# Kernel tuning notes

Measured on AMD Instinct MI355X. Metric: run time of the kernel, lower is better.

## Reference

```python
import jax, jax.numpy as jnp
import numpy as np

N = 50000
E = 800000
DIM_IN = 128
DIM_H = 16
HEADS = 8
DIM_OUT = 16
NEG_SLOPE = 0.2


def setup_inputs() -> dict:
    key = jax.random.key(0)
    ks = jax.random.split(key, 12)
    def glorot(k, shape):
        fan_in = shape[0]
        return jax.random.normal(k, shape, dtype=jnp.float32) / np.sqrt(fan_in)
    x = jax.random.normal(ks[0], (N, DIM_IN), dtype=jnp.float32)
    edge_index = jax.random.randint(ks[1], (2, E), 0, N, dtype=jnp.int64)
    # layer 1: GATv2Conv(dim_in, dim_h, heads=8)
    Wl1 = glorot(ks[2], (DIM_IN, HEADS * DIM_H))
    Wr1 = glorot(ks[3], (DIM_IN, HEADS * DIM_H))
    att1 = glorot(ks[4], (HEADS, DIM_H))
    bias1 = jnp.zeros((HEADS * DIM_H,), dtype=jnp.float32)
    # layer 2: GATv2Conv(dim_h*heads, dim_out, heads=1)
    Wl2 = glorot(ks[5], (HEADS * DIM_H, DIM_OUT))
    Wr2 = glorot(ks[6], (HEADS * DIM_H, DIM_OUT))
    att2 = glorot(ks[7], (1, DIM_OUT))
    bias2 = jnp.zeros((DIM_OUT,), dtype=jnp.float32)
    return {"x": x, "edge_index": edge_index, "Wl1": Wl1, "Wr1": Wr1,
            "att1": att1, "bias1": bias1, "Wl2": Wl2, "Wr2": Wr2,
            "att2": att2, "bias2": bias2}


def gatv2_layer(x, src, dst, Wl, Wr, att, bias, n_nodes, heads, ch):
    # x: [N, F_in]; src/dst: [Etot] (self-loops included)
    xl = (x @ Wl).reshape(n_nodes, heads, ch)  # source transform
    xr = (x @ Wr).reshape(n_nodes, heads, ch)  # target transform
    e = jax.nn.leaky_relu(xl[src] + xr[dst], NEG_SLOPE)      # [Etot, H, C]
    logits = jnp.einsum('ehc,hc->eh', e, att)                # [Etot, H]
    # segment softmax over incoming edges of each target node
    m = jax.ops.segment_max(logits, dst, num_segments=n_nodes)
    a = jnp.exp(logits - m[dst])
    denom = jax.ops.segment_sum(a, dst, num_segments=n_nodes)
    alpha = a / denom[dst]                                   # [Etot, H]
    out = jax.ops.segment_sum(xl[src] * alpha[:, :, None], dst,
                              num_segments=n_nodes)          # [N, H, C]
    return out.reshape(n_nodes, heads * ch) + bias


def reference(x, edge_index, Wl1, Wr1, att1, bias1, Wl2, Wr2, att2, bias2):
    # PyG GATv2Conv adds self-loops by default
    loops = jnp.arange(N, dtype=edge_index.dtype)
    src = jnp.concatenate([edge_index[0], loops])
    dst = jnp.concatenate([edge_index[1], loops])
    # dropout is identity in eval mode
    h = gatv2_layer(x, src, dst, Wl1, Wr1, att1, bias1, N, HEADS, DIM_H)
    h = jax.nn.elu(h)
    h = gatv2_layer(h, src, dst, Wl2, Wr2, att2, bias2, N, 1, DIM_OUT)
    return h, jax.nn.log_softmax(h, axis=1)
```

## Files before the change

### kernel.cpp

```cpp
#include <hip/hip_runtime.h>
#include <hip/hip_bf16.h>
#include <math.h>

#define NN 50000
#define EE 800000
#define DIN 128
#define HEADS 8
#define DH 16
#define DOUT 16
#define NEG 0.2f
#define GM 32
#define GB ((NN + GM - 1) / GM)
#define NB ((NN + 255) / 256)
#define DEGB ((EE / 4 + 255) / 256)
#define NPART 8
#define RANGE (NN / NPART)
#define FILLB (DEGB * NPART)
#define PAD 64

typedef __attribute__((ext_vector_type(8))) short bf16x8;
typedef __attribute__((ext_vector_type(4))) float f32x4;
typedef __attribute__((ext_vector_type(4))) int i32x4;

__device__ __forceinline__ unsigned pack2bf(float a, float b) {
    union { __hip_bfloat162 h; unsigned u; } c;
    c.h = __float22bfloat162_rn(make_float2(a, b));
    return c.u;
}
__device__ __forceinline__ unsigned short f2bf(float v) {
    union { __hip_bfloat16 h; unsigned short u; } c;
    c.h = __float2bfloat16(v);
    return c.u;
}
__device__ __forceinline__ float bflo(unsigned u) { return __uint_as_float(u << 16); }
__device__ __forceinline__ float bfhi(unsigned u) { return __uint_as_float(u & 0xffff0000u); }

__global__ __launch_bounds__(256) void init_wcvt(int* __restrict__ cnt,
                                                 unsigned short* __restrict__ esrcPad,
                                                 const float* __restrict__ Wl,
                                                 const float* __restrict__ Wr,
                                                 unsigned short* __restrict__ Wb,
                                                 const float* __restrict__ Wl2,
                                                 const float* __restrict__ Wr2,
                                                 unsigned short* __restrict__ Wb2) {
    int b = blockIdx.x, t = threadIdx.x;
    if (b < NB) {
        int i = b * 256 + t;
        if (i < NN) {
            cnt[i] = 1;
            esrcPad[(size_t)i * PAD] = (unsigned short)i;
        }
    } else if (b < NB + 128) {
        int i = (b - NB) * 256 + t;
        int n = i >> 7, k = i & 127;
        float v = (n < 128) ? Wl[k * 128 + n] : Wr[k * 128 + (n - 128)];
        Wb[i] = f2bf(v);
    } else {
        int i = (b - NB - 128) * 256 + t;
        int n = i >> 7, k = i & 127;
        float v = (n < 16) ? Wl2[k * 16 + n] : Wr2[k * 16 + (n - 16)];
        Wb2[i] = f2bf(v);
    }
}

__global__ __launch_bounds__(256) void fill_gemm1(const int* __restrict__ ei,
                                                  int* __restrict__ cnt,
                                                  unsigned short* __restrict__ esrcPad,
                                                  const float* __restrict__ x,
                                                  const unsigned short* __restrict__ Wb,
                                                  unsigned short* __restrict__ xlb,
                                                  float* __restrict__ xr) {
    __shared__ unsigned short As[GM][136];
    int t = threadIdx.x;
    if (blockIdx.x < FILLB) {
        int chunk = blockIdx.x >> 3;
        int r = blockIdx.x & 7;
        int i = chunk * 256 + t;
        if (i >= EE / 4) return;
        i32x4 ss = __builtin_nontemporal_load(((const i32x4*)ei) + i);
        i32x4 dd = __builtin_nontemporal_load(((const i32x4*)(ei + EE)) + i);
        int lo = r * RANGE;
        int p;
        if ((unsigned)(dd[0] - lo) < RANGE) {
            p = atomicAdd(&cnt[dd[0]], 1);
            esrcPad[(size_t)dd[0] * PAD + p] = (unsigned short)ss[0];
        }
        if ((unsigned)(dd[1] - lo) < RANGE) {
            p = atomicAdd(&cnt[dd[1]], 1);
            esrcPad[(size_t)dd[1] * PAD + p] = (unsigned short)ss[1];
        }
        if ((unsigned)(dd[2] - lo) < RANGE) {
            p = atomicAdd(&cnt[dd[2]], 1);
            esrcPad[(size_t)dd[2] * PAD + p] = (unsigned short)ss[2];
        }
        if ((unsigned)(dd[3] - lo) < RANGE) {
            p = atomicAdd(&cnt[dd[3]], 1);
            esrcPad[(size_t)dd[3] * PAD + p] = (unsigned short)ss[3];
        }
        return;
    }
    int n0 = (blockIdx.x - FILLB) * GM;
    {
        int row = t >> 3, seg = t & 7;
        int nsrc = n0 + row < NN ? n0 + row : NN - 1;
        const f32x4* xp = (const f32x4*)(x + (size_t)nsrc * DIN + 16 * seg);
        f32x4 v0 = __builtin_nontemporal_load(xp);
        f32x4 v1 = __builtin_nontemporal_load(xp + 1);
        f32x4 v2 = __builtin_nontemporal_load(xp + 2);
        f32x4 v3 = __builtin_nontemporal_load(xp + 3);
        uint4 p0 = make_uint4(pack2bf(v0[0], v0[1]), pack2bf(v0[2], v0[3]),
                              pack2bf(v1[0], v1[1]), pack2bf(v1[2], v1[3]));
        uint4 p1 = make_uint4(pack2bf(v2[0], v2[1]), pack2bf(v2[2], v2[3]),
                              pack2bf(v3[0], v3[1]), pack2bf(v3[2], v3[3]));
        *(uint4*)&As[row][16 * seg]     = p0;
        *(uint4*)&As[row][16 * seg + 8] = p1;
    }
    __syncthreads();
    int lane = t & 63, w = t >> 6;
    int m = lane & 15, quad = lane >> 4;
    f32x4 acc[2][4];
#pragma unroll
    for (int mt = 0; mt < 2; ++mt)
#pragma unroll
        for (int nt = 0; nt < 4; ++nt) acc[mt][nt] = (f32x4){0.f, 0.f, 0.f, 0.f};
#pragma unroll
    for (int ks = 0; ks < 4; ++ks) {
        int k = 32 * ks + 8 * quad;
        bf16x8 a0 = *(const bf16x8*)&As[m][k];
        bf16x8 a1 = *(const bf16x8*)&As[16 + m][k];
#pragma unroll
        for (int nt = 0; nt < 4; ++nt) {
            int n = 64 * w + 16 * nt + m;
            bf16x8 b = *(const bf16x8*)(Wb + (size_t)n * 128 + k);
            acc[0][nt] = __builtin_amdgcn_mfma_f32_16x16x32_bf16(a0, b, acc[0][nt], 0, 0, 0);
            acc[1][nt] = __builtin_amdgcn_mfma_f32_16x16x32_bf16(a1, b, acc[1][nt], 0, 0, 0);
        }
    }
#pragma unroll
    for (int mt = 0; mt < 2; ++mt) {
#pragma unroll
        for (int nt = 0; nt < 4; ++nt) {
            int col = 64 * w + 16 * nt + m;
            int rbase = n0 + 16 * mt + 4 * quad;
            if (col < 128) {
#pragma unroll
                for (int r = 0; r < 4; ++r) {
                    int row = rbase + r;
                    if (row < NN) xlb[(size_t)row * DIN + col] = f2bf(acc[mt][nt][r]);
                }
            } else {
#pragma unroll
                for (int r = 0; r < 4; ++r) {
                    int row = rbase + r;
                    if (row < NN) xr[(size_t)row * DIN + (col - 128)] = acc[mt][nt][r];
                }
            }
        }
    }
}

__global__ __launch_bounds__(256) void l1_fused(const unsigned short* __restrict__ esrcPad,
                                                const int* __restrict__ cnt,
                                                const unsigned short* __restrict__ xlb,
                                                const float* __restrict__ xr,
                                                const float* __restrict__ att,
                                                const float* __restrict__ bias,
                                                unsigned short* __restrict__ hb) {
    int d = blockIdx.x * 4 + (threadIdx.x >> 6);
    int lane = threadIdx.x & 63;
    int quarter = lane >> 4;
    int q16 = lane & 15;
    int rs = d * PAD;
    int re = rs + cnt[d];
    int last = re - 1;
    float4 xr0 = ((const float4*)(xr + (size_t)d * DIN))[2 * q16];
    float4 xr1 = ((const float4*)(xr + (size_t)d * DIN))[2 * q16 + 1];
    float4 at0 = ((const float4*)att)[2 * q16];
    float4 at1 = ((const float4*)att)[2 * q16 + 1];
    float4 a0 = make_float4(0.f, 0.f, 0.f, 0.f);
    float4 a1 = make_float4(0.f, 0.f, 0.f, 0.f);
    float l = 0.f;
    int slot = rs + quarter;
    int c0 = slot < last ? slot : last;
    int s0 = esrcPad[c0];
    int c1 = slot + 4 < last ? slot + 4 : last;
    int s1 = esrcPad[c1];
    uint4 row = ((const uint4*)(xlb + (size_t)s0 * DIN))[q16];
    for (; slot < re; slot += 4) {
        uint4 cur = row;
        int c2 = slot + 8 < last ? slot + 8 : last;
        int s2 = esrcPad[c2];
        row = ((const uint4*)(xlb + (size_t)s1 * DIN))[q16];
        s1 = s2;
        float f0 = bflo(cur.x), f1 = bfhi(cur.x);
        float f2 = bflo(cur.y), f3 = bfhi(cur.y);
        float f4 = bflo(cur.z), f5 = bfhi(cur.z);
        float f6 = bflo(cur.w), f7 = bfhi(cur.w);
        float v0 = f0 + xr0.x; v0 = fmaxf(v0, NEG * v0);
        float v1 = f1 + xr0.y; v1 = fmaxf(v1, NEG * v1);
        float v2 = f2 + xr0.z; v2 = fmaxf(v2, NEG * v2);
        float v3 = f3 + xr0.w; v3 = fmaxf(v3, NEG * v3);
        float v4 = f4 + xr1.x; v4 = fmaxf(v4, NEG * v4);
        float v5 = f5 + xr1.y; v5 = fmaxf(v5, NEG * v5);
        float v6 = f6 + xr1.z; v6 = fmaxf(v6, NEG * v6);
        float v7 = f7 + xr1.w; v7 = fmaxf(v7, NEG * v7);
        float w = at0.x * v0 + at0.y * v1 + at0.z * v2 + at0.w * v3
                + at1.x * v4 + at1.y * v5 + at1.z * v6 + at1.w * v7;
        w += __shfl_xor(w, 1);
        float p = __expf(w);
        a0.x += p * f0; a0.y += p * f1; a0.z += p * f2; a0.w += p * f3;
        a1.x += p * f4; a1.y += p * f5; a1.z += p * f6; a1.w += p * f7;
        l += p;
    }
#pragma unroll
    for (int off = 16; off < 64; off <<= 1) {
        a0.x += __shfl_xor(a0.x, off); a0.y += __shfl_xor(a0.y, off);
        a0.z += __shfl_xor(a0.z, off); a0.w += __shfl_xor(a0.w, off);
        a1.x += __shfl_xor(a1.x, off); a1.y += __shfl_xor(a1.y, off);
        a1.z += __shfl_xor(a1.z, off); a1.w += __shfl_xor(a1.w, off);
        l += __shfl_xor(l, off);
    }
    if (quarter == 0) {
        float inv = 1.f / l;
        float4 b0 = ((const float4*)bias)[2 * q16];
        float4 b1 = ((const float4*)bias)[2 * q16 + 1];
        float4 o0, o1;
        o0.x = a0.x * inv + b0.x; o0.x = o0.x > 0.f ? o0.x : expm1f(o0.x);
        o0.y = a0.y * inv + b0.y; o0.y = o0.y > 0.f ? o0.y : expm1f(o0.y);
        o0.z = a0.z * inv + b0.z; o0.z = o0.z > 0.f ? o0.z : expm1f(o0.z);
        o0.w = a0.w * inv + b0.w; o0.w = o0.w > 0.f ? o0.w : expm1f(o0.w);
        o1.x = a1.x * inv + b1.x; o1.x = o1.x > 0.f ? o1.x : expm1f(o1.x);
        o1.y = a1.y * inv + b1.y; o1.y = o1.y > 0.f ? o1.y : expm1f(o1.y);
        o1.z = a1.z * inv + b1.z; o1.z = o1.z > 0.f ? o1.z : expm1f(o1.z);
        o1.w = a1.w * inv + b1.w; o1.w = o1.w > 0.f ? o1.w : expm1f(o1.w);
        uint4 pk = make_uint4(pack2bf(o0.x, o0.y), pack2bf(o0.z, o0.w),
                              pack2bf(o1.x, o1.y), pack2bf(o1.z, o1.w));
        ((uint4*)(hb + (size_t)d * DIN))[q16] = pk;
    }
}

__global__ __launch_bounds__(256) void gemm2(const unsigned short* __restrict__ hb,
                                             const unsigned short* __restrict__ Wb2,
                                             float* __restrict__ xl2, float* __restrict__ xr2) {
    __shared__ unsigned short As[GM][136];
    int t = threadIdx.x;
    int n0 = blockIdx.x * GM;
    {
        int row = t >> 3, s8 = t & 7;
        int nsrc = n0 + row < NN ? n0 + row : NN - 1;
        const uint4* src = (const uint4*)(hb + (size_t)nsrc * DIN);
        *(uint4*)&As[row][8 * s8]      = src[s8];
        *(uint4*)&As[row][8 * s8 + 64] = src[s8 + 8];
    }
    __syncthreads();
    int lane = t & 63, w = t >> 6;
    int m = lane & 15, quad = lane >> 4;
    int mt = w & 1, nt = w >> 1;
    f32x4 acc = (f32x4){0.f, 0.f, 0.f, 0.f};
#pragma unroll
    for (int ks = 0; ks < 4; ++ks) {
        int k = 32 * ks + 8 * quad;
        bf16x8 a = *(const bf16x8*)&As[16 * mt + m][k];
        bf16x8 b = *(const bf16x8*)(Wb2 + (size_t)(16 * nt + m) * 128 + k);
        acc = __builtin_amdgcn_mfma_f32_16x16x32_bf16(a, b, acc, 0, 0, 0);
    }
    float* __restrict__ dst = (nt == 0) ? xl2 : xr2;
#pragma unroll
    for (int r = 0; r < 4; ++r) {
        int node = n0 + 16 * mt + 4 * quad + r;
        if (node < NN) dst[(size_t)node * DOUT + m] = acc[r];
    }
}

__global__ __launch_bounds__(256) void l2_fused(const unsigned short* __restrict__ esrcPad,
                                                const int* __restrict__ cnt,
                                                const float* __restrict__ xl,
                                                const float* __restrict__ xr,
                                                const float* __restrict__ att,
                                                const float* __restrict__ bias,
                                                float* __restrict__ out) {
    int d = blockIdx.x * 4 + (threadIdx.x >> 6);
    int lane = threadIdx.x & 63;
    int sl = lane >> 2;
    int q = lane & 3;
    int rs = d * PAD;
    int re = rs + cnt[d];
    int last = re - 1;
    float4 xrq = ((const float4*)(xr + (size_t)d * DOUT))[q];
    float4 atq = ((const float4*)att)[q];
    float4 acc = make_float4(0.f, 0.f, 0.f, 0.f);
    float l = 0.f;
    int slot = rs + sl;
    int c0 = slot < last ? slot : last;
    int s0 = esrcPad[c0];
    for (; slot < re; slot += 16) {
        int c1 = slot + 16 < last ? slot + 16 : last;
        int s1 = esrcPad[c1];
        float4 cur = ((const float4*)(xl + (size_t)s0 * DOUT))[q];
        s0 = s1;
        float v0 = cur.x + xrq.x; v0 = fmaxf(v0, NEG * v0);
        float v1 = cur.y + xrq.y; v1 = fmaxf(v1, NEG * v1);
        float v2 = cur.z + xrq.z; v2 = fmaxf(v2, NEG * v2);
        float v3 = cur.w + xrq.w; v3 = fmaxf(v3, NEG * v3);
        float w = atq.x * v0 + atq.y * v1 + atq.z * v2 + atq.w * v3;
        w += __shfl_xor(w, 1);
        w += __shfl_xor(w, 2);
        float p = __expf(w);
        acc.x += p * cur.x; acc.y += p * cur.y;
        acc.z += p * cur.z; acc.w += p * cur.w;
        l += p;
    }
#pragma unroll
    for (int off = 4; off < 64; off <<= 1) {
        acc.x += __shfl_xor(acc.x, off);
        acc.y += __shfl_xor(acc.y, off);
        acc.z += __shfl_xor(acc.z, off);
        acc.w += __shfl_xor(acc.w, off);
        l += __shfl_xor(l, off);
    }
    float inv = 1.f / l;
    float4 b = ((const float4*)bias)[q];
    float4 v;
    v.x = acc.x * inv + b.x; v.y = acc.y * inv + b.y;
    v.z = acc.z * inv + b.z; v.w = acc.w * inv + b.w;
    float m = fmaxf(fmaxf(v.x, v.y), fmaxf(v.z, v.w));
    m = fmaxf(m, __shfl_xor(m, 1));
    m = fmaxf(m, __shfl_xor(m, 2));
    float es = __expf(v.x - m) + __expf(v.y - m) + __expf(v.z - m) + __expf(v.w - m);
    es += __shfl_xor(es, 1);
    es += __shfl_xor(es, 2);
    float lse = m + __logf(es);
    if (sl == 0) {
        ((float4*)(out + (size_t)d * DOUT))[q] = v;
        float4 ls;
        ls.x = v.x - lse; ls.y = v.y - lse; ls.z = v.z - lse; ls.w = v.w - lse;
        ((float4*)(out + (size_t)NN * DOUT + (size_t)d * DOUT))[q] = ls;
    }
}

extern "C" void kernel_launch(void* const* d_in, const int* in_sizes, int n_in,
                              void* d_out, int out_size, void* d_ws, size_t ws_size,
                              hipStream_t stream) {
    const float* x     = (const float*)d_in[0];
    const int*   ei    = (const int*)d_in[1];
    const float* Wl1   = (const float*)d_in[2];
    const float* Wr1   = (const float*)d_in[3];
    const float* att1  = (const float*)d_in[4];
    const float* bias1 = (const float*)d_in[5];
    const float* Wl2   = (const float*)d_in[6];
    const float* Wr2   = (const float*)d_in[7];
    const float* att2  = (const float*)d_in[8];
    const float* bias2 = (const float*)d_in[9];
    float* out = (float*)d_out;

    float* xr1    = (float*)d_ws;
    float* xl2    = xr1 + (size_t)NN * DIN;
    float* xr2    = xl2 + (size_t)NN * DOUT;
    unsigned short* xlb = (unsigned short*)(xr2 + (size_t)NN * DOUT);
    unsigned short* hb  = xlb + (size_t)NN * DIN;
    unsigned short* Wb  = hb + (size_t)NN * DIN;
    unsigned short* Wb2 = Wb + 256 * 128;
    unsigned short* esrcPad = Wb2 + 32 * 128;
    int*   cnt    = (int*)(esrcPad + (size_t)NN * PAD);

    const int B = 256;
    init_wcvt<<<NB + 144, B, 0, stream>>>(cnt, esrcPad, Wl1, Wr1, Wb, Wl2, Wr2, Wb2);
    fill_gemm1<<<FILLB + GB, B, 0, stream>>>(ei, cnt, esrcPad, x, Wb, xlb, xr1);

    l1_fused<<<NN / 4, B, 0, stream>>>(esrcPad, cnt, xlb, xr1, att1, bias1, hb);

    gemm2<<<GB, B, 0, stream>>>(hb, Wb2, xl2, xr2);

    l2_fused<<<NN / 4, B, 0, stream>>>(esrcPad, cnt, xl2, xr2, att2, bias2, out);
}
```

Baseline: 232.8 us.

## Bucket edges by destination partition before scattering into padded adjacency

Replaces the 8-way redundant edge read in the fill kernel with a single pass that bins edges by destination range into per-partition buckets, using shared-memory counting and one global atomic per bucket per block. A new scatter kernel then processes each partition's bucket, so blocks interleaved across partitions touch a localized slice of the count and adjacency arrays. The layer kernels remap block indices the same way, interleaving the partitions. This cuts the repeated edge-list traffic but adds a kernel launch, bucket write and read traffic, and fixed bucket capacities that assume a roughly uniform destination distribution.

After: 237.2 us. Within noise of the previous version (+1.9%).

```diff
diff --git a/kernel.cpp b/kernel.cpp
--- a/kernel.cpp
+++ b/kernel.cpp
@@ -12,10 +12,12 @@
 #define GM 32
 #define GB ((NN + GM - 1) / GM)
 #define NB ((NN + 255) / 256)
-#define DEGB ((EE / 4 + 255) / 256)
+#define ABLK ((EE / 4 + 255) / 256)
 #define NPART 8
 #define RANGE (NN / NPART)
-#define FILLB (DEGB * NPART)
+#define RB 1563
+#define SCATB 64
+#define BUCKCAP 110000
 #define PAD 64
 
 typedef __attribute__((ext_vector_type(8))) short bf16x8;
@@ -36,7 +38,7 @@
 __device__ __forceinline__ float bfhi(unsigned u) { return __uint_as_float(u & 0xffff0000u); }
 
 __global__ __launch_bounds__(256) void init_wcvt(int* __restrict__ cnt,
-                                                 unsigned short* __restrict__ esrcPad,
+                                                 unsigned* __restrict__ bhead,
                                                  const float* __restrict__ Wl,
                                                  const float* __restrict__ Wr,
                                                  unsigned short* __restrict__ Wb,
@@ -44,12 +46,10 @@
                                                  const float* __restrict__ Wr2,
                                                  unsigned short* __restrict__ Wb2) {
     int b = blockIdx.x, t = threadIdx.x;
+    if (b == 0 && t < 8) bhead[t] = 0;
     if (b < NB) {
         int i = b * 256 + t;
-        if (i < NN) {
-            cnt[i] = 1;
-            esrcPad[(size_t)i * PAD] = (unsigned short)i;
-        }
+        if (i < NN) cnt[i] = 1;
     } else if (b < NB + 128) {
         int i = (b - NB) * 256 + t;
         int n = i >> 7, k = i & 127;
@@ -64,42 +64,62 @@
 }
 
 __global__ __launch_bounds__(256) void fill_gemm1(const int* __restrict__ ei,
-                                                  int* __restrict__ cnt,
-                                                  unsigned short* __restrict__ esrcPad,
+                                                  unsigned* __restrict__ bhead,
+                                                  unsigned* __restrict__ bucket,
                                                   const float* __restrict__ x,
                                                   const unsigned short* __restrict__ Wb,
                                                   unsigned short* __restrict__ xlb,
                                                   float* __restrict__ xr) {
     __shared__ unsigned short As[GM][136];
     int t = threadIdx.x;
-    if (blockIdx.x < FILLB) {
-        int chunk = blockIdx.x >> 3;
-        int r = blockIdx.x & 7;
-        int i = chunk * 256 + t;
-        if (i >= EE / 4) return;
-        i32x4 ss = __builtin_nontemporal_load(((const i32x4*)ei) + i);
-        i32x4 dd = __builtin_nontemporal_load(((const i32x4*)(ei + EE)) + i);
-        int lo = r * RANGE;
-        int p;
-        if ((unsigned)(dd[0] - lo) < RANGE) {
-            p = atomicAdd(&cnt[dd[0]], 1);
-            esrcPad[(size_t)dd[0] * PAD + p] = (unsigned short)ss[0];
-        }
-        if ((unsigned)(dd[1] - lo) < RANGE) {
-            p = atomicAdd(&cnt[dd[1]], 1);
-            esrcPad[(size_t)dd[1] * PAD + p] = (unsigned short)ss[1];
-        }
-        if ((unsigned)(dd[2] - lo) < RANGE) {
-            p = atomicAdd(&cnt[dd[2]], 1);
-            esrcPad[(size_t)dd[2] * PAD + p] = (unsigned short)ss[2];
-        }
-        if ((unsigned)(dd[3] - lo) < RANGE) {
-            p = atomicAdd(&cnt[dd[3]], 1);
-            esrcPad[(size_t)dd[3] * PAD + p] = (unsigned short)ss[3];
+    if (blockIdx.x < ABLK) {
+        unsigned* lrec = (unsigned*)&As[0][0];
+        unsigned* lcnt = lrec + 1024;
+        unsigned* loff = lcnt + 8;
+        unsigned* lpos = loff + 8;
+        unsigned* gbase = lpos + 8;
+        int i = blockIdx.x * 256 + t;
+        bool valid = i < EE / 4;
+        i32x4 ss, dd;
+        unsigned bb[4];
+        if (valid) {
+            ss = __builtin_nontemporal_load(((const i32x4*)ei) + i);
+            dd = __builtin_nontemporal_load(((const i32x4*)(ei + EE)) + i);
+        }
+        if (t < 8) { lcnt[t] = 0; lpos[t] = 0; }
+        __syncthreads();
+        if (valid) {
+#pragma unroll
+            for (int e = 0; e < 4; ++e) {
+                bb[e] = (unsigned)dd[e] / RANGE;
+                atomicAdd(&lcnt[bb[e]], 1u);
+            }
+        }
+        __syncthreads();
+        if (t == 0) {
+            unsigned run = 0;
+#pragma unroll
+            for (int q = 0; q < 8; ++q) { loff[q] = run; run += lcnt[q]; }
+        }
+        if (t < 8 && lcnt[t] > 0) gbase[t] = atomicAdd(&bhead[t], lcnt[t]);
+        __syncthreads();
+        if (valid) {
+#pragma unroll
+            for (int e = 0; e < 4; ++e) {
+                unsigned p = atomicAdd(&lpos[bb[e]], 1u);
+                lrec[loff[bb[e]] + p] = ((unsigned)ss[e] << 16) | (unsigned)dd[e];
+            }
+        }
+        __syncthreads();
+        unsigned total = loff[7] + lcnt[7];
+        for (unsigned j = t; j < total; j += 256) {
+            unsigned q = 0;
+            while (q < 7 && j >= loff[q + 1]) ++q;
+            bucket[(size_t)q * BUCKCAP + gbase[q] + (j - loff[q])] = lrec[j];
         }
         return;
     }
-    int n0 = (blockIdx.x - FILLB) * GM;
+    int n0 = (blockIdx.x - ABLK) * GM;
     {
         int row = t >> 3, seg = t & 7;
         int nsrc = n0 + row < NN ? n0 + row : NN - 1;
@@ -159,6 +179,28 @@
     }
 }
 
+__global__ __launch_bounds__(256) void scatter_b(const unsigned* __restrict__ bucket,
+                                                 const unsigned* __restrict__ bhead,
+                                                 int* __restrict__ cnt,
+                                                 unsigned short* __restrict__ esrcPad) {
+    int r = blockIdx.x & 7;
+    int g = blockIdx.x >> 3;
+    int t = threadIdx.x;
+    if (g == 0) {
+        for (int dq = t; dq < RANGE; dq += 256) {
+            int d = r * RANGE + dq;
+            esrcPad[(size_t)d * PAD] = (unsigned short)d;
+        }
+    }
+    unsigned n = bhead[r];
+    for (unsigned i = (unsigned)g * 256 + t; i < n; i += SCATB * 256) {
+        unsigned rec = __builtin_nontemporal_load(bucket + (size_t)r * BUCKCAP + i);
+        unsigned s = rec >> 16, d = rec & 0xffffu;
+        int p = atomicAdd(&cnt[d], 1);
+        esrcPad[(size_t)d * PAD + p] = (unsigned short)s;
+    }
+}
+
 __global__ __launch_bounds__(256) void l1_fused(const unsigned short* __restrict__ esrcPad,
                                                 const int* __restrict__ cnt,
                                                 const unsigned short* __restrict__ xlb,
@@ -166,7 +208,10 @@
                                                 const float* __restrict__ att,
                                                 const float* __restrict__ bias,
                                                 unsigned short* __restrict__ hb) {
-    int d = blockIdx.x * 4 + (threadIdx.x >> 6);
+    int r = blockIdx.x & 7;
+    int dq = (blockIdx.x >> 3) * 4 + (threadIdx.x >> 6);
+    if (dq >= RANGE) return;
+    int d = r * RANGE + dq;
     int lane = threadIdx.x & 63;
     int quarter = lane >> 4;
     int q16 = lane & 15;
@@ -279,7 +324,10 @@
                                                 const float* __restrict__ att,
                                                 const float* __restrict__ bias,
                                                 float* __restrict__ out) {
-    int d = blockIdx.x * 4 + (threadIdx.x >> 6);
+    int r = blockIdx.x & 7;
+    int dq = (blockIdx.x >> 3) * 4 + (threadIdx.x >> 6);
+    if (dq >= RANGE) return;
+    int d = r * RANGE + dq;
     int lane = threadIdx.x & 63;
     int sl = lane >> 2;
     int q = lane & 3;
@@ -362,14 +410,17 @@
     unsigned short* Wb2 = Wb + 256 * 128;
     unsigned short* esrcPad = Wb2 + 32 * 128;
     int*   cnt    = (int*)(esrcPad + (size_t)NN * PAD);
+    unsigned* bucket = (unsigned*)(cnt + NN);
+    unsigned* bhead  = bucket + (size_t)8 * BUCKCAP;
 
     const int B = 256;
-    init_wcvt<<<NB + 144, B, 0, stream>>>(cnt, esrcPad, Wl1, Wr1, Wb, Wl2, Wr2, Wb2);
-    fill_gemm1<<<FILLB + GB, B, 0, stream>>>(ei, cnt, esrcPad, x, Wb, xlb, xr1);
-
-    l1_fused<<<NN / 4, B, 0, stream>>>(esrcPad, cnt, xlb, xr1, att1, bias1, hb);
+    init_wcvt<<<NB + 144, B, 0, stream>>>(cnt, bhead, Wl1, Wr1, Wb, Wl2, Wr2, Wb2);
+    fill_gemm1<<<ABLK + GB, B, 0, stream>>>(ei, bhead, bucket, x, Wb, xlb, xr1);
+    scatter_b<<<NPART * SCATB, B, 0, stream>>>(bucket, bhead, cnt, esrcPad);
+
+    l1_fused<<<NPART * RB, B, 0, stream>>>(esrcPad, cnt, xlb, xr1, att1, bias1, hb);
 
     gemm2<<<GB, B, 0, stream>>>(hb, Wb2, xl2, xr2);
 
-    l2_fused<<<NN / 4, B, 0, stream>>>(esrcPad, cnt, xl2, xr2, att2, bias2, out);
-}
+    l2_fused<<<NPART * RB, B, 0, stream>>>(esrcPad, cnt, xl2, xr2, att2, bias2, out);
+}
```
